# Optimization experiments

Hardware: AMD Instinct MI355X
Metric: run time of the kernel (lower is better)

Reference implementation:

```python
import jax, jax.numpy as jnp
import numpy as np

N = 100000
E = 1600000
IN_C, HID_C, OUT_C = 128, 64, 64
NEG_SLOPE = 0.2


def setup_inputs() -> dict:
    key = jax.random.key(0)
    ks = jax.random.split(key, 12)
    x = jax.random.normal(ks[0], (N, IN_C), dtype=jnp.float32)
    edge_index = jax.random.randint(ks[1], (2, E), 0, N, dtype=jnp.int64)
    s = 0.1
    # layer 1: heads=2, out=HID_C, concat=True
    W1 = jax.random.normal(ks[2], (IN_C, 2 * HID_C), dtype=jnp.float32) * s
    a_src1 = jax.random.normal(ks[3], (2, HID_C), dtype=jnp.float32) * s
    a_dst1 = jax.random.normal(ks[4], (2, HID_C), dtype=jnp.float32) * s
    b1 = jnp.zeros((2 * HID_C,), dtype=jnp.float32)
    # layer 2: heads=1, out=OUT_C, concat=False
    W2 = jax.random.normal(ks[5], (2 * HID_C, OUT_C), dtype=jnp.float32) * s
    a_src2 = jax.random.normal(ks[6], (1, OUT_C), dtype=jnp.float32) * s
    a_dst2 = jax.random.normal(ks[7], (1, OUT_C), dtype=jnp.float32) * s
    b2 = jnp.zeros((OUT_C,), dtype=jnp.float32)
    return {"x": x, "edge_index": edge_index, "W1": W1, "a_src1": a_src1,
            "a_dst1": a_dst1, "b1": b1, "W2": W2, "a_src2": a_src2,
            "a_dst2": a_dst2, "b2": b2}


def gat_conv(x, src, dst, W, a_src, a_dst, bias, heads, out_ch, concat):
    n = x.shape[0]
    h = (x @ W).reshape(n, heads, out_ch)            # [N,H,C]
    alpha_s = jnp.einsum('nhc,hc->nh', h, a_src)     # [N,H]
    alpha_d = jnp.einsum('nhc,hc->nh', h, a_dst)
    e = jax.nn.leaky_relu(alpha_s[src] + alpha_d[dst], NEG_SLOPE)  # [E,H]
    emax = jax.ops.segment_max(e, dst, num_segments=n)
    e = jnp.exp(e - emax[dst])
    denom = jax.ops.segment_sum(e, dst, num_segments=n)
    alpha = e / (denom[dst] + 1e-16)                 # edge softmax over dst
    out = jax.ops.segment_sum(h[src] * alpha[:, :, None], dst, num_segments=n)
    out = out.reshape(n, heads * out_ch) if concat else out.mean(axis=1)
    return out + bias


def reference(x, edge_index, W1, a_src1, a_dst1, b1, W2, a_src2, a_dst2, b2):
    # PyG GATConv adds self-loops by default; append once (same graph both layers)
    loop = jnp.arange(N, dtype=edge_index.dtype)
    src = jnp.concatenate([edge_index[0], loop])
    dst = jnp.concatenate([edge_index[1], loop])
    h = jax.nn.elu(gat_conv(x, src, dst, W1, a_src1, a_dst1, b1, 2, HID_C, True))
    out = jax.nn.elu(gat_conv(h, src, dst, W2, a_src2, a_dst2, b2, 1, OUT_C, False))
    return out
```

## Files before the change

### kernel.cpp

```cpp
#include <hip/hip_runtime.h>
#include <hip/hip_bf16.h>
#include <math.h>

#define N_NODES 100000
#define N_EDGES 1600000
#define TOT_E   (N_EDGES + N_NODES)
#define NBG     ((N_NODES + 127) / 128)
#define NBC     ((TOT_E + 255) / 256)

__device__ __forceinline__ float lrelu(float v){ return v > 0.f ? v : 0.2f * v; }
__device__ __forceinline__ float elu_(float v){ return v > 0.f ? v : expm1f(v); }
__device__ __forceinline__ ushort f2bf(float f){
  unsigned u = __float_as_uint(f);
  u = (u + 0x7FFFu + ((u >> 16) & 1u)) >> 16;
  return (ushort)u;
}
__device__ __forceinline__ float bf2f(ushort u){
  return __uint_as_float(((unsigned)u) << 16);
}
__device__ __forceinline__ float bflo(unsigned p){ return __uint_as_float(p << 16); }
__device__ __forceinline__ float bfhi(unsigned p){ return __uint_as_float(p & 0xffff0000u); }

__global__ __launch_bounds__(256) void k_gc(const float* __restrict__ x, const float* __restrict__ W,
                                            const float* __restrict__ a_src, const float* __restrict__ a_dst,
                                            ushort* __restrict__ h, float* __restrict__ as1,
                                            float* __restrict__ ad1,
                                            const int* __restrict__ ei, int* __restrict__ cnt,
                                            const float* __restrict__ W2, const float* __restrict__ a_src2,
                                            const float* __restrict__ a_dst2, float* __restrict__ vs,
                                            float* __restrict__ vd, int n){
  __shared__ float sx[128][36];
  __shared__ float sw[32][132];

  if (blockIdx.x >= NBG){
    if (blockIdx.x < NBG + NBC){
      int i = (blockIdx.x - NBG) * 256 + threadIdx.x;
      if (i < TOT_E){
        int d = (i < N_EDGES) ? ei[N_EDGES + i] : (i - N_EDGES);
        atomicAdd(&cnt[d], 1);
      }
    } else {
      int k = threadIdx.x;
      if (k < 128){
        float s = 0.f, d = 0.f;
        for (int c = 0; c < 64; ++c){
          float w = W2[k * 64 + c];
          s = fmaf(w, a_src2[c], s);
          d = fmaf(w, a_dst2[c], d);
        }
        vs[k] = s; vd[k] = d;
      }
    }
    return;
  }

  const int tid  = threadIdx.x;
  const int cg   = tid & 7;
  const int slot = tid >> 3;
  const int rbase = blockIdx.x * 128;
  const int r0   = rbase + slot * 4;
  const int col0 = cg * 16;

  float acc[4][16] = {};

  for (int kc = 0; kc < 4; ++kc){
    __syncthreads();
    #pragma unroll
    for (int i = 0; i < 4; ++i){
      int f   = tid + 256 * i;
      int row = f >> 3;
      int c4  = f & 7;
      int gr  = rbase + row; if (gr > n - 1) gr = n - 1;
      float4 v = *(const float4*)(x + (size_t)gr * 128 + kc * 32 + c4 * 4);
      *(float4*)(&sx[row][c4 * 4]) = v;
    }
    #pragma unroll
    for (int i = 0; i < 4; ++i){
      int f  = tid + 256 * i;
      int k  = f >> 5;
      int c4 = f & 31;
      float4 v = *(const float4*)(W + (size_t)(kc * 32 + k) * 128 + c4 * 4);
      *(float4*)(&sw[k][c4 * 4]) = v;
    }
    __syncthreads();

    #pragma unroll 8
    for (int j = 0; j < 32; ++j){
      float4 w0 = *(const float4*)(&sw[j][col0]);
      float4 w1 = *(const float4*)(&sw[j][col0 + 4]);
      float4 w2 = *(const float4*)(&sw[j][col0 + 8]);
      float4 w3 = *(const float4*)(&sw[j][col0 + 12]);
      #pragma unroll
      for (int i = 0; i < 4; ++i){
        float xv = sx[slot * 4 + i][j];
        acc[i][0]  = fmaf(xv, w0.x, acc[i][0]);  acc[i][1]  = fmaf(xv, w0.y, acc[i][1]);
        acc[i][2]  = fmaf(xv, w0.z, acc[i][2]);  acc[i][3]  = fmaf(xv, w0.w, acc[i][3]);
        acc[i][4]  = fmaf(xv, w1.x, acc[i][4]);  acc[i][5]  = fmaf(xv, w1.y, acc[i][5]);
        acc[i][6]  = fmaf(xv, w1.z, acc[i][6]);  acc[i][7]  = fmaf(xv, w1.w, acc[i][7]);
        acc[i][8]  = fmaf(xv, w2.x, acc[i][8]);  acc[i][9]  = fmaf(xv, w2.y, acc[i][9]);
        acc[i][10] = fmaf(xv, w2.z, acc[i][10]); acc[i][11] = fmaf(xv, w2.w, acc[i][11]);
        acc[i][12] = fmaf(xv, w3.x, acc[i][12]); acc[i][13] = fmaf(xv, w3.y, acc[i][13]);
        acc[i][14] = fmaf(xv, w3.z, acc[i][14]); acc[i][15] = fmaf(xv, w3.w, acc[i][15]);
      }
    }
  }

  #pragma unroll
  for (int i = 0; i < 4; ++i){
    int r = r0 + i;
    float sp = 0.f, dp = 0.f;
    #pragma unroll
    for (int j = 0; j < 16; ++j){
      sp = fmaf(acc[i][j], a_src[col0 + j], sp);
      dp = fmaf(acc[i][j], a_dst[col0 + j], dp);
    }
    float s0 = (col0 < 64) ? sp : 0.f, s1 = (col0 < 64) ? 0.f : sp;
    float d0 = (col0 < 64) ? dp : 0.f, d1 = (col0 < 64) ? 0.f : dp;
    #pragma unroll
    for (int m = 1; m <= 4; m <<= 1){
      s0 += __shfl_xor(s0, m); s1 += __shfl_xor(s1, m);
      d0 += __shfl_xor(d0, m); d1 += __shfl_xor(d1, m);
    }
    if (r < n){
      union { uint4 q[2]; ushort us[16]; } pk;
      #pragma unroll
      for (int j = 0; j < 16; ++j) pk.us[j] = f2bf(acc[i][j]);
      uint4* dst = (uint4*)(h + (size_t)r * 128 + col0);
      dst[0] = pk.q[0]; dst[1] = pk.q[1];
      if (cg == 0){
        as1[2 * r] = s0; as1[2 * r + 1] = s1;
        ad1[2 * r] = d0; ad1[2 * r + 1] = d1;
      }
    }
  }
}

__global__ __launch_bounds__(1024) void k_scan1(const int* __restrict__ cnt, int* __restrict__ off,
                                                int* __restrict__ bs){
  __shared__ int s[1024];
  int t = threadIdx.x;
  int i = blockIdx.x * 1024 + t;
  int v = (i < N_NODES) ? cnt[i] : 0;
  s[t] = v;
  __syncthreads();
  for (int o = 1; o < 1024; o <<= 1){
    int tmp = 0;
    if (t >= o) tmp = s[t - o];
    __syncthreads();
    if (t >= o) s[t] += tmp;
    __syncthreads();
  }
  if (i < N_NODES) off[i] = s[t] - v;
  if (t == 1023) bs[blockIdx.x] = s[1023];
}

__global__ __launch_bounds__(128) void k_scan2(int* __restrict__ bs, int* __restrict__ off, int nb){
  __shared__ int s[128];
  int t = threadIdx.x;
  int v = (t < nb) ? bs[t] : 0;
  s[t] = v;
  __syncthreads();
  #pragma unroll
  for (int o = 1; o < 128; o <<= 1){
    int tmp = 0;
    if (t >= o) tmp = s[t - o];
    __syncthreads();
    if (t >= o) s[t] += tmp;
    __syncthreads();
  }
  if (t < nb) bs[t] = s[t] - v;
  if (t == nb - 1) off[N_NODES] = s[t];
}

__global__ __launch_bounds__(1024) void k_scan3(int* __restrict__ off, int* __restrict__ cur,
                                                const int* __restrict__ bs){
  int i = blockIdx.x * 1024 + threadIdx.x;
  if (i < N_NODES){
    int v = off[i] + bs[blockIdx.x];
    off[i] = v;
    cur[i] = v;
  }
}

__global__ __launch_bounds__(256) void k_fill_w(const int* __restrict__ ei, int* __restrict__ cur,
                                                uint4* __restrict__ csr4,
                                                const float* __restrict__ as1, const float* __restrict__ ad1){
  int i = blockIdx.x * 256 + threadIdx.x;
  if (i >= TOT_E) return;
  int s, d;
  if (i < N_EDGES){ s = ei[i]; d = ei[N_EDGES + i]; }
  else            { s = d = i - N_EDGES; }
  int p = atomicAdd(&cur[d], 1);
  float2 a  = *(const float2*)(as1 + 2u * (unsigned)s);
  float2 ad = *(const float2*)(ad1 + 2u * (unsigned)d);
  uint4 v;
  v.x = (unsigned)s;
  v.y = __float_as_uint(__expf(lrelu(a.x + ad.x)));
  v.z = __float_as_uint(__expf(lrelu(a.y + ad.y)));
  v.w = (unsigned)d;
  csr4[p] = v;
}

__global__ __launch_bounds__(256) void k_ew2(const uint4* __restrict__ csr4,
                                             const float* __restrict__ as2, const float* __restrict__ ad2,
                                             uint2* __restrict__ ew){
  int i = blockIdx.x * 256 + threadIdx.x;
  if (i >= TOT_E) return;
  uint4 v = csr4[i];
  float w = __expf(lrelu(as2[v.x] + ad2[v.w]));
  ew[i] = make_uint2(v.x, __float_as_uint(w));
}

__global__ __launch_bounds__(256) void k_agg1(const int* __restrict__ off, const uint4* __restrict__ csr4,
                                              const ushort* __restrict__ h,
                                              const float* __restrict__ b,
                                              const float* __restrict__ vs2, const float* __restrict__ vd2,
                                              const float* __restrict__ W2,
                                              ushort* __restrict__ z, float* __restrict__ as2,
                                              float* __restrict__ ad2){
  __shared__ float yly[4][128];
  int wid  = threadIdx.x >> 6;
  int node = blockIdx.x * 4 + wid;
  int lane = threadIdx.x & 63;
  int head = lane >> 5;
  int c0   = lane * 2;
  int s0 = off[node], e0 = off[node + 1];

  float acc0 = 0.f, acc1 = 0.f, den = 0.f;
  int k = s0;
  for (; k + 7 < e0; k += 8){
    int ku = __builtin_amdgcn_readfirstlane(k);
    uint4 eA = csr4[ku],     eB = csr4[ku + 1], eC = csr4[ku + 2], eD = csr4[ku + 3];
    uint4 eE = csr4[ku + 4], eF = csr4[ku + 5], eG = csr4[ku + 6], eH = csr4[ku + 7];
    unsigned hA = *(const unsigned*)(h + ((size_t)eA.x << 7) + c0);
    unsigned hB = *(const unsigned*)(h + ((size_t)eB.x << 7) + c0);
    unsigned hC = *(const unsigned*)(h + ((size_t)eC.x << 7) + c0);
    unsigned hD = *(const unsigned*)(h + ((size_t)eD.x << 7) + c0);
    unsigned hE = *(const unsigned*)(h + ((size_t)eE.x << 7) + c0);
    unsigned hF = *(const unsigned*)(h + ((size_t)eF.x << 7) + c0);
    unsigned hG = *(const unsigned*)(h + ((size_t)eG.x << 7) + c0);
    unsigned hH = *(const unsigned*)(h + ((size_t)eH.x << 7) + c0);
    float wA = __uint_as_float(head ? eA.z : eA.y);
    float wB = __uint_as_float(head ? eB.z : eB.y);
    float wC = __uint_as_float(head ? eC.z : eC.y);
    float wD = __uint_as_float(head ? eD.z : eD.y);
    float wE = __uint_as_float(head ? eE.z : eE.y);
    float wF = __uint_as_float(head ? eF.z : eF.y);
    float wG = __uint_as_float(head ? eG.z : eG.y);
    float wH = __uint_as_float(head ? eH.z : eH.y);
    den += ((wA + wB) + (wC + wD)) + ((wE + wF) + (wG + wH));
    acc0 = fmaf(wA, bflo(hA), acc0); acc1 = fmaf(wA, bfhi(hA), acc1);
    acc0 = fmaf(wB, bflo(hB), acc0); acc1 = fmaf(wB, bfhi(hB), acc1);
    acc0 = fmaf(wC, bflo(hC), acc0); acc1 = fmaf(wC, bfhi(hC), acc1);
    acc0 = fmaf(wD, bflo(hD), acc0); acc1 = fmaf(wD, bfhi(hD), acc1);
    acc0 = fmaf(wE, bflo(hE), acc0); acc1 = fmaf(wE, bfhi(hE), acc1);
    acc0 = fmaf(wF, bflo(hF), acc0); acc1 = fmaf(wF, bfhi(hF), acc1);
    acc0 = fmaf(wG, bflo(hG), acc0); acc1 = fmaf(wG, bfhi(hG), acc1);
    acc0 = fmaf(wH, bflo(hH), acc0); acc1 = fmaf(wH, bfhi(hH), acc1);
  }
  if (k + 3 < e0){
    int ku = __builtin_amdgcn_readfirstlane(k);
    uint4 eA = csr4[ku],     eB = csr4[ku + 1], eC = csr4[ku + 2], eD = csr4[ku + 3];
    unsigned hA = *(const unsigned*)(h + ((size_t)eA.x << 7) + c0);
    unsigned hB = *(const unsigned*)(h + ((size_t)eB.x << 7) + c0);
    unsigned hC = *(const unsigned*)(h + ((size_t)eC.x << 7) + c0);
    unsigned hD = *(const unsigned*)(h + ((size_t)eD.x << 7) + c0);
    float wA = __uint_as_float(head ? eA.z : eA.y);
    float wB = __uint_as_float(head ? eB.z : eB.y);
    float wC = __uint_as_float(head ? eC.z : eC.y);
    float wD = __uint_as_float(head ? eD.z : eD.y);
    den += (wA + wB) + (wC + wD);
    acc0 = fmaf(wA, bflo(hA), acc0); acc1 = fmaf(wA, bfhi(hA), acc1);
    acc0 = fmaf(wB, bflo(hB), acc0); acc1 = fmaf(wB, bfhi(hB), acc1);
    acc0 = fmaf(wC, bflo(hC), acc0); acc1 = fmaf(wC, bfhi(hC), acc1);
    acc0 = fmaf(wD, bflo(hD), acc0); acc1 = fmaf(wD, bfhi(hD), acc1);
    k += 4;
  }
  for (; k < e0; ++k){
    int ku = __builtin_amdgcn_readfirstlane(k);
    uint4 eA = csr4[ku];
    unsigned hA = *(const unsigned*)(h + ((size_t)eA.x << 7) + c0);
    float wA = __uint_as_float(head ? eA.z : eA.y);
    den += wA;
    acc0 = fmaf(wA, bflo(hA), acc0); acc1 = fmaf(wA, bfhi(hA), acc1);
  }

  float inv = 1.f / (den + 1e-16f);
  float o0 = elu_(acc0 * inv + b[c0]);
  float o1 = elu_(acc1 * inv + b[c0 + 1]);

  *(float2*)(&yly[wid][c0]) = make_float2(o0, o1);

  float s2 = fmaf(o0, vs2[c0], o1 * vs2[c0 + 1]);
  float d2 = fmaf(o0, vd2[c0], o1 * vd2[c0 + 1]);
  #pragma unroll
  for (int m = 32; m; m >>= 1){ s2 += __shfl_xor(s2, m); d2 += __shfl_xor(d2, m); }
  if (lane == 0){ as2[node] = s2; ad2[node] = d2; }

  asm volatile("s_waitcnt lgkmcnt(0)" ::: "memory");

  float zacc = 0.f;
  const float* yw = yly[wid];
  #pragma unroll 4
  for (int q = 0; q < 32; ++q){
    float4 yv = *(const float4*)(yw + 4 * q);
    const float* wr = W2 + (q * 4) * 64 + lane;
    zacc = fmaf(yv.x, wr[0],   zacc);
    zacc = fmaf(yv.y, wr[64],  zacc);
    zacc = fmaf(yv.z, wr[128], zacc);
    zacc = fmaf(yv.w, wr[192], zacc);
  }
  z[((unsigned)node << 6) + lane] = f2bf(zacc);
}

__global__ __launch_bounds__(256) void k_agg2(const int* __restrict__ off, const uint2* __restrict__ ew,
                                              const ushort* __restrict__ z,
                                              const float* __restrict__ b2, float* __restrict__ out){
  int node = blockIdx.x * 4 + (threadIdx.x >> 6);
  int lane = threadIdx.x & 63;
  int s0 = off[node], e0 = off[node + 1];

  float acc = 0.f, den = 0.f;
  int k = s0;
  for (; k + 7 < e0; k += 8){
    int ku = __builtin_amdgcn_readfirstlane(k);
    uint2 eA = ew[ku],     eB = ew[ku + 1], eC = ew[ku + 2], eD = ew[ku + 3];
    uint2 eE = ew[ku + 4], eF = ew[ku + 5], eG = ew[ku + 6], eH = ew[ku + 7];
    ushort zA = z[((size_t)eA.x << 6) + lane];
    ushort zB = z[((size_t)eB.x << 6) + lane];
    ushort zC = z[((size_t)eC.x << 6) + lane];
    ushort zD = z[((size_t)eD.x << 6) + lane];
    ushort zE = z[((size_t)eE.x << 6) + lane];
    ushort zF = z[((size_t)eF.x << 6) + lane];
    ushort zG = z[((size_t)eG.x << 6) + lane];
    ushort zH = z[((size_t)eH.x << 6) + lane];
    float wA = __uint_as_float(eA.y), wB = __uint_as_float(eB.y);
    float wC = __uint_as_float(eC.y), wD = __uint_as_float(eD.y);
    float wE = __uint_as_float(eE.y), wF = __uint_as_float(eF.y);
    float wG = __uint_as_float(eG.y), wH = __uint_as_float(eH.y);
    den += ((wA + wB) + (wC + wD)) + ((wE + wF) + (wG + wH));
    acc = fmaf(wA, bf2f(zA), acc); acc = fmaf(wB, bf2f(zB), acc);
    acc = fmaf(wC, bf2f(zC), acc); acc = fmaf(wD, bf2f(zD), acc);
    acc = fmaf(wE, bf2f(zE), acc); acc = fmaf(wF, bf2f(zF), acc);
    acc = fmaf(wG, bf2f(zG), acc); acc = fmaf(wH, bf2f(zH), acc);
  }
  if (k + 3 < e0){
    int ku = __builtin_amdgcn_readfirstlane(k);
    uint2 eA = ew[ku], eB = ew[ku + 1], eC = ew[ku + 2], eD = ew[ku + 3];
    ushort zA = z[((size_t)eA.x << 6) + lane];
    ushort zB = z[((size_t)eB.x << 6) + lane];
    ushort zC = z[((size_t)eC.x << 6) + lane];
    ushort zD = z[((size_t)eD.x << 6) + lane];
    float wA = __uint_as_float(eA.y), wB = __uint_as_float(eB.y);
    float wC = __uint_as_float(eC.y), wD = __uint_as_float(eD.y);
    den += (wA + wB) + (wC + wD);
    acc = fmaf(wA, bf2f(zA), acc); acc = fmaf(wB, bf2f(zB), acc);
    acc = fmaf(wC, bf2f(zC), acc); acc = fmaf(wD, bf2f(zD), acc);
    k += 4;
  }
  for (; k < e0; ++k){
    int ku = __builtin_amdgcn_readfirstlane(k);
    uint2 eA = ew[ku];
    ushort zA = z[((size_t)eA.x << 6) + lane];
    float wA = __uint_as_float(eA.y);
    den += wA;
    acc = fmaf(wA, bf2f(zA), acc);
  }

  float inv = 1.f / (den + 1e-16f);
  out[((unsigned)node << 6) + lane] = elu_(acc * inv + b2[lane]);
}

extern "C" void kernel_launch(void* const* d_in, const int* in_sizes, int n_in,
                              void* d_out, int out_size, void* d_ws, size_t ws_size,
                              hipStream_t stream){
  const float* x      = (const float*)d_in[0];
  const int*   ei     = (const int*)d_in[1];
  const float* W1     = (const float*)d_in[2];
  const float* a_src1 = (const float*)d_in[3];
  const float* a_dst1 = (const float*)d_in[4];
  const float* b1     = (const float*)d_in[5];
  const float* W2     = (const float*)d_in[6];
  const float* a_src2 = (const float*)d_in[7];
  const float* a_dst2 = (const float*)d_in[8];
  const float* b2     = (const float*)d_in[9];
  float* out = (float*)d_out;

  char* ws = (char*)d_ws;
  size_t o = 0;
  auto alloc = [&](size_t bytes){ size_t r = o; o = (o + bytes + 255) & ~(size_t)255; return r; };
  int*    tmpN = (int*)(ws + alloc((size_t)N_NODES * 4));
  int*    bs   = (int*)(ws + alloc(512));
  int*    off  = (int*)(ws + alloc((size_t)(N_NODES + 1) * 4));
  uint4*  csr4 = (uint4*)(ws + alloc((size_t)TOT_E * 16));
  uint2*  ew   = (uint2*)(ws + alloc((size_t)TOT_E * 8));
  float*  as1  = (float*)(ws + alloc((size_t)N_NODES * 2 * 4));
  float*  ad1  = (float*)(ws + alloc((size_t)N_NODES * 2 * 4));
  float*  as2  = (float*)(ws + alloc((size_t)N_NODES * 4));
  float*  ad2  = (float*)(ws + alloc((size_t)N_NODES * 4));
  float*  vs2  = (float*)(ws + alloc(512));
  float*  vd2  = (float*)(ws + alloc(512));
  ushort* z    = (ushort*)(ws + alloc((size_t)N_NODES * 64 * 2));
  ushort* h1   = (ushort*)d_out;
  (void)ws_size; (void)in_sizes; (void)n_in; (void)out_size;

  const int nblk_edges = NBC;
  const int nblk_scan  = (N_NODES + 1023) / 1024;
  const int nblk_wave4 = N_NODES / 4;

  hipMemsetAsync(tmpN, 0, (size_t)N_NODES * 4, stream);

  k_gc<<<NBG + NBC + 1, 256, 0, stream>>>(x, W1, a_src1, a_dst1, h1, as1, ad1,
                                          ei, tmpN, W2, a_src2, a_dst2, vs2, vd2, N_NODES);

  k_scan1 <<<nblk_scan, 1024, 0, stream>>>(tmpN, off, bs);
  k_scan2 <<<1, 128, 0, stream>>>(bs, off, nblk_scan);
  k_scan3 <<<nblk_scan, 1024, 0, stream>>>(off, tmpN, bs);
  k_fill_w<<<nblk_edges, 256, 0, stream>>>(ei, tmpN, csr4, as1, ad1);

  k_agg1 <<<nblk_wave4, 256, 0, stream>>>(off, csr4, h1, b1, vs2, vd2, W2, z, as2, ad2);

  k_ew2  <<<nblk_edges, 256, 0, stream>>>(csr4, as2, ad2, ew);
  k_agg2 <<<nblk_wave4, 256, 0, stream>>>(off, ew, z, b2, out);
}
```

Baseline: 374.4 us.

## Compute layer-1 attention logits via folded W·a vectors and fuse GEMM with CSR fill

Layer-1 attention scores are now computed directly from x using precomputed W1·a_src and W1·a_dst vectors in a front kernel, alongside degree counting. Because the scores no longer depend on the GEMM output, the dense x@W1 projection moves to a later kernel that also performs the CSR fill. The GEMM and the edge scatter can then overlap in one launch, and one kernel launch is removed. In exchange, x is read twice and the scores are summed in a different order, which can change rounding slightly.

```diff
diff --git a/kernel.cpp b/kernel.cpp
--- a/kernel.cpp
+++ b/kernel.cpp
@@ -7,6 +7,7 @@
 #define TOT_E   (N_EDGES + N_NODES)
 #define NBG     ((N_NODES + 127) / 128)
 #define NBC     ((TOT_E + 255) / 256)
+#define NBA     800
 
 __device__ __forceinline__ float lrelu(float v){ return v > 0.f ? v : 0.2f * v; }
 __device__ __forceinline__ float elu_(float v){ return v > 0.f ? v : expm1f(v); }
@@ -21,35 +22,138 @@
 __device__ __forceinline__ float bflo(unsigned p){ return __uint_as_float(p << 16); }
 __device__ __forceinline__ float bfhi(unsigned p){ return __uint_as_float(p & 0xffff0000u); }
 
-__global__ __launch_bounds__(256) void k_gc(const float* __restrict__ x, const float* __restrict__ W,
-                                            const float* __restrict__ a_src, const float* __restrict__ a_dst,
-                                            ushort* __restrict__ h, float* __restrict__ as1,
-                                            float* __restrict__ ad1,
-                                            const int* __restrict__ ei, int* __restrict__ cnt,
-                                            const float* __restrict__ W2, const float* __restrict__ a_src2,
-                                            const float* __restrict__ a_dst2, float* __restrict__ vs,
-                                            float* __restrict__ vd, int n){
+__global__ __launch_bounds__(256) void k_front(const float* __restrict__ x, const float* __restrict__ W1,
+                                               const float* __restrict__ a_src1, const float* __restrict__ a_dst1,
+                                               const int* __restrict__ ei, int* __restrict__ cnt,
+                                               const float* __restrict__ W2, const float* __restrict__ a_src2,
+                                               const float* __restrict__ a_dst2, float* __restrict__ vs2,
+                                               float* __restrict__ vd2,
+                                               float* __restrict__ as1, float* __restrict__ ad1){
+  __shared__ float vls[2][128], vld[2][128];
+  int bid = blockIdx.x;
+  if (bid < NBA){
+    for (int item = threadIdx.x; item < 512; item += 256){
+      int vec = item >> 7;
+      int k   = item & 127;
+      int hd  = vec & 1;
+      bool isS = vec < 2;
+      const float* av = (isS ? a_src1 : a_dst1) + hd * 64;
+      const float* wr = W1 + k * 128 + hd * 64;
+      float acc = 0.f;
+      #pragma unroll 8
+      for (int c = 0; c < 64; ++c) acc = fmaf(wr[c], av[c], acc);
+      if (isS) vls[hd][k] = acc; else vld[hd][k] = acc;
+    }
+    __syncthreads();
+    int wv = threadIdx.x >> 6;
+    int lane = threadIdx.x & 63;
+    int nend = bid * 125 + 125;
+    for (int n = bid * 125 + wv; n < nend; n += 4){
+      float2 xv = *(const float2*)(x + (size_t)n * 128 + lane * 2);
+      float s0 = fmaf(xv.x, vls[0][lane*2], xv.y * vls[0][lane*2+1]);
+      float s1 = fmaf(xv.x, vls[1][lane*2], xv.y * vls[1][lane*2+1]);
+      float d0 = fmaf(xv.x, vld[0][lane*2], xv.y * vld[0][lane*2+1]);
+      float d1 = fmaf(xv.x, vld[1][lane*2], xv.y * vld[1][lane*2+1]);
+      #pragma unroll
+      for (int m = 32; m; m >>= 1){
+        s0 += __shfl_xor(s0, m); s1 += __shfl_xor(s1, m);
+        d0 += __shfl_xor(d0, m); d1 += __shfl_xor(d1, m);
+      }
+      if (lane == 0){
+        as1[2*n] = s0; as1[2*n+1] = s1;
+        ad1[2*n] = d0; ad1[2*n+1] = d1;
+      }
+    }
+  } else if (bid < NBA + NBC){
+    int i = (bid - NBA) * 256 + threadIdx.x;
+    if (i < TOT_E){
+      int d = (i < N_EDGES) ? ei[N_EDGES + i] : (i - N_EDGES);
+      atomicAdd(&cnt[d], 1);
+    }
+  } else {
+    int k = threadIdx.x;
+    if (k < 128){
+      float s = 0.f, d = 0.f;
+      for (int c = 0; c < 64; ++c){
+        float w = W2[k * 64 + c];
+        s = fmaf(w, a_src2[c], s);
+        d = fmaf(w, a_dst2[c], d);
+      }
+      vs2[k] = s; vd2[k] = d;
+    }
+  }
+}
+
+__global__ __launch_bounds__(1024) void k_scan1(const int* __restrict__ cnt, int* __restrict__ off,
+                                                int* __restrict__ bs){
+  __shared__ int s[1024];
+  int t = threadIdx.x;
+  int i = blockIdx.x * 1024 + t;
+  int v = (i < N_NODES) ? cnt[i] : 0;
+  s[t] = v;
+  __syncthreads();
+  for (int o = 1; o < 1024; o <<= 1){
+    int tmp = 0;
+    if (t >= o) tmp = s[t - o];
+    __syncthreads();
+    if (t >= o) s[t] += tmp;
+    __syncthreads();
+  }
+  if (i < N_NODES) off[i] = s[t] - v;
+  if (t == 1023) bs[blockIdx.x] = s[1023];
+}
+
+__global__ __launch_bounds__(128) void k_scan2(int* __restrict__ bs, int* __restrict__ off, int nb){
+  __shared__ int s[128];
+  int t = threadIdx.x;
+  int v = (t < nb) ? bs[t] : 0;
+  s[t] = v;
+  __syncthreads();
+  #pragma unroll
+  for (int o = 1; o < 128; o <<= 1){
+    int tmp = 0;
+    if (t >= o) tmp = s[t - o];
+    __syncthreads();
+    if (t >= o) s[t] += tmp;
+    __syncthreads();
+  }
+  if (t < nb) bs[t] = s[t] - v;
+  if (t == nb - 1) off[N_NODES] = s[t];
+}
+
+__global__ __launch_bounds__(1024) void k_scan3(int* __restrict__ off, int* __restrict__ cur,
+                                                const int* __restrict__ bs){
+  int i = blockIdx.x * 1024 + threadIdx.x;
+  if (i < N_NODES){
+    int v = off[i] + bs[blockIdx.x];
+    off[i] = v;
+    cur[i] = v;
+  }
+}
+
+__global__ __launch_bounds__(256) void k_back(const float* __restrict__ x, const float* __restrict__ W,
+                                              ushort* __restrict__ h, int n,
+                                              const int* __restrict__ ei, int* __restrict__ cur,
+                                              uint4* __restrict__ csr4,
+                                              const float* __restrict__ as1, const float* __restrict__ ad1){
   __shared__ float sx[128][36];
   __shared__ float sw[32][132];
 
   if (blockIdx.x >= NBG){
-    if (blockIdx.x < NBG + NBC){
-      int i = (blockIdx.x - NBG) * 256 + threadIdx.x;
-      if (i < TOT_E){
-        int d = (i < N_EDGES) ? ei[N_EDGES + i] : (i - N_EDGES);
-        atomicAdd(&cnt[d], 1);
-      }
-    } else {
-      int k = threadIdx.x;
-      if (k < 128){
-        float s = 0.f, d = 0.f;
-        for (int c = 0; c < 64; ++c){
-          float w = W2[k * 64 + c];
-          s = fmaf(w, a_src2[c], s);
-          d = fmaf(w, a_dst2[c], d);
-        }
-        vs[k] = s; vd[k] = d;
-      }
+    int i = (blockIdx.x - NBG) * 256 + threadIdx.x;
+    if (i < TOT_E){
+      int s, d;
+      if (i < N_EDGES){ s = ei[i]; d = ei[N_EDGES + i]; }
+      else            { s = d = i - N_EDGES; }
+      int p = atomicAdd(&cur[d], 1);
+      float2 a  = *(const float2*)(as1 + 2u * (unsigned)s);
+      float2 ad = *(const float2*)(ad1 + 2u * (unsigned)d);
+      uint4 v;
+      v.x = (unsigned)s;
+      v.y = __float_as_uint(__expf(lrelu(a.x + ad.x)));
+      v.z = __float_as_uint(__expf(lrelu(a.y + ad.y)));
+      v.w = (unsigned)d;
+      csr4[p] = v;
     }
     return;
   }
@@ -108,97 +212,14 @@
   #pragma unroll
   for (int i = 0; i < 4; ++i){
     int r = r0 + i;
-    float sp = 0.f, dp = 0.f;
-    #pragma unroll
-    for (int j = 0; j < 16; ++j){
-      sp = fmaf(acc[i][j], a_src[col0 + j], sp);
-      dp = fmaf(acc[i][j], a_dst[col0 + j], dp);
-    }
-    float s0 = (col0 < 64) ? sp : 0.f, s1 = (col0 < 64) ? 0.f : sp;
-    float d0 = (col0 < 64) ? dp : 0.f, d1 = (col0 < 64) ? 0.f : dp;
-    #pragma unroll
-    for (int m = 1; m <= 4; m <<= 1){
-      s0 += __shfl_xor(s0, m); s1 += __shfl_xor(s1, m);
-      d0 += __shfl_xor(d0, m); d1 += __shfl_xor(d1, m);
-    }
     if (r < n){
       union { uint4 q[2]; ushort us[16]; } pk;
       #pragma unroll
       for (int j = 0; j < 16; ++j) pk.us[j] = f2bf(acc[i][j]);
       uint4* dst = (uint4*)(h + (size_t)r * 128 + col0);
       dst[0] = pk.q[0]; dst[1] = pk.q[1];
-      if (cg == 0){
-        as1[2 * r] = s0; as1[2 * r + 1] = s1;
-        ad1[2 * r] = d0; ad1[2 * r + 1] = d1;
-      }
-    }
-  }
-}
-
-__global__ __launch_bounds__(1024) void k_scan1(const int* __restrict__ cnt, int* __restrict__ off,
-                                                int* __restrict__ bs){
-  __shared__ int s[1024];
-  int t = threadIdx.x;
-  int i = blockIdx.x * 1024 + t;
-  int v = (i < N_NODES) ? cnt[i] : 0;
-  s[t] = v;
-  __syncthreads();
-  for (int o = 1; o < 1024; o <<= 1){
-    int tmp = 0;
-    if (t >= o) tmp = s[t - o];
-    __syncthreads();
-    if (t >= o) s[t] += tmp;
-    __syncthreads();
-  }
-  if (i < N_NODES) off[i] = s[t] - v;
-  if (t == 1023) bs[blockIdx.x] = s[1023];
-}
-
-__global__ __launch_bounds__(128) void k_scan2(int* __restrict__ bs, int* __restrict__ off, int nb){
-  __shared__ int s[128];
-  int t = threadIdx.x;
-  int v = (t < nb) ? bs[t] : 0;
-  s[t] = v;
-  __syncthreads();
-  #pragma unroll
-  for (int o = 1; o < 128; o <<= 1){
-    int tmp = 0;
-    if (t >= o) tmp = s[t - o];
-    __syncthreads();
-    if (t >= o) s[t] += tmp;
-    __syncthreads();
-  }
-  if (t < nb) bs[t] = s[t] - v;
-  if (t == nb - 1) off[N_NODES] = s[t];
-}
-
-__global__ __launch_bounds__(1024) void k_scan3(int* __restrict__ off, int* __restrict__ cur,
-                                                const int* __restrict__ bs){
-  int i = blockIdx.x * 1024 + threadIdx.x;
-  if (i < N_NODES){
-    int v = off[i] + bs[blockIdx.x];
-    off[i] = v;
-    cur[i] = v;
-  }
-}
-
-__global__ __launch_bounds__(256) void k_fill_w(const int* __restrict__ ei, int* __restrict__ cur,
-                                                uint4* __restrict__ csr4,
-                                                const float* __restrict__ as1, const float* __restrict__ ad1){
-  int i = blockIdx.x * 256 + threadIdx.x;
-  if (i >= TOT_E) return;
-  int s, d;
-  if (i < N_EDGES){ s = ei[i]; d = ei[N_EDGES + i]; }
-  else            { s = d = i - N_EDGES; }
-  int p = atomicAdd(&cur[d], 1);
-  float2 a  = *(const float2*)(as1 + 2u * (unsigned)s);
-  float2 ad = *(const float2*)(ad1 + 2u * (unsigned)d);
-  uint4 v;
-  v.x = (unsigned)s;
-  v.y = __float_as_uint(__expf(lrelu(a.x + ad.x)));
-  v.z = __float_as_uint(__expf(lrelu(a.y + ad.y)));
-  v.w = (unsigned)d;
-  csr4[p] = v;
+    }
+  }
 }
 
 __global__ __launch_bounds__(256) void k_ew2(const uint4* __restrict__ csr4,
@@ -404,22 +425,22 @@
   ushort* h1   = (ushort*)d_out;
   (void)ws_size; (void)in_sizes; (void)n_in; (void)out_size;
 
-  const int nblk_edges = NBC;
   const int nblk_scan  = (N_NODES + 1023) / 1024;
   const int nblk_wave4 = N_NODES / 4;
 
   hipMemsetAsync(tmpN, 0, (size_t)N_NODES * 4, stream);
 
-  k_gc<<<NBG + NBC + 1, 256, 0, stream>>>(x, W1, a_src1, a_dst1, h1, as1, ad1,
-                                          ei, tmpN, W2, a_src2, a_dst2, vs2, vd2, N_NODES);
-
-  k_scan1 <<<nblk_scan, 1024, 0, stream>>>(tmpN, off, bs);
-  k_scan2 <<<1, 128, 0, stream>>>(bs, off, nblk_scan);
-  k_scan3 <<<nblk_scan, 1024, 0, stream>>>(off, tmpN, bs);
-  k_fill_w<<<nblk_edges, 256, 0, stream>>>(ei, tmpN, csr4, as1, ad1);
-
-  k_agg1 <<<nblk_wave4, 256, 0, stream>>>(off, csr4, h1, b1, vs2, vd2, W2, z, as2, ad2);
-
-  k_ew2  <<<nblk_edges, 256, 0, stream>>>(csr4, as2, ad2, ew);
-  k_agg2 <<<nblk_wave4, 256, 0, stream>>>(off, ew, z, b2, out);
-}
+  k_front<<<NBA + NBC + 1, 256, 0, stream>>>(x, W1, a_src1, a_dst1, ei, tmpN,
+                                             W2, a_src2, a_dst2, vs2, vd2, as1, ad1);
+
+  k_scan1<<<nblk_scan, 1024, 0, stream>>>(tmpN, off, bs);
+  k_scan2<<<1, 128, 0, stream>>>(bs, off, nblk_scan);
+  k_scan3<<<nblk_scan, 1024, 0, stream>>>(off, tmpN, bs);
+
+  k_back<<<NBG + NBC, 256, 0, stream>>>(x, W1, h1, N_NODES, ei, tmpN, csr4, as1, ad1);
+
+  k_agg1<<<nblk_wave4, 256, 0, stream>>>(off, csr4, h1, b1, vs2, vd2, W2, z, as2, ad2);
+
+  k_ew2 <<<(TOT_E + 255) / 256, 256, 0, stream>>>(csr4, as2, ad2, ew);
+  k_agg2<<<nblk_wave4, 256, 0, stream>>>(off, ew, z, b2, out);
+}
```

After: 407.9 us. 1.09x slower.
